# Performance work log

Measured on AMD Instinct MI355X. Metric: run time of the kernel, lower is better.

The kernel has to match this reference:

```python
import jax, jax.numpy as jnp
import numpy as np

B, T, HID = 8, 1024, 1024
N_HEADS, HEAD = 16, HID // 16
MAX_F, BASE = 1024, 10000.0


def _rope_tables():
    inv_freq = 1.0 / (BASE ** (np.arange(0, HEAD, 2, dtype=np.float32) / HEAD))
    t = np.arange(MAX_F, dtype=np.float32)
    freqs = np.einsum('i,j->ij', t, inv_freq)  # (MAX_F, HEAD/2)
    emb = np.concatenate([freqs, freqs], axis=-1)  # (MAX_F, HEAD)
    return jnp.asarray(np.cos(emb)), jnp.asarray(np.sin(emb))


def setup_inputs() -> dict:
    key = jax.random.key(0)
    ks = jax.random.split(key, 6)
    x = jax.random.normal(ks[0], (B, T, HID), dtype=jnp.float32)
    Wq = jax.random.normal(ks[1], (HID, HID), dtype=jnp.float32) * 0.02
    Wk = jax.random.normal(ks[2], (HID, HID), dtype=jnp.float32) * 0.02
    Wv = jax.random.normal(ks[3], (HID, HID), dtype=jnp.float32) * 0.02
    Wo = jax.random.normal(ks[4], (HID, HID), dtype=jnp.float32) * 0.02
    cos, sin = _rope_tables()
    attn_mask = jnp.ones((B, T, T), dtype=jnp.int32)
    timestamp = jax.random.randint(ks[5], (B, T), 0, MAX_F, dtype=jnp.int32)
    return {"x": x, "Wq": Wq, "Wk": Wk, "Wv": Wv, "Wo": Wo,
            "cos": cos, "sin": sin, "attn_mask": attn_mask, "timestamp": timestamp}


def _rotate_half(u):
    u1, u2 = u[..., : HEAD // 2], u[..., HEAD // 2:]
    return jnp.concatenate([-u2, u1], axis=-1)


def reference(x, Wq, Wk, Wv, Wo, cos, sin, attn_mask, timestamp):
    Bx, Tx, _ = x.shape
    # QKV projections (nn.Linear: x @ W.T), reshape to (B, H, T, head)
    def proj(W):
        return (x @ W.T).reshape(Bx, Tx, N_HEADS, HEAD).transpose(0, 2, 1, 3)
    q, k, v = proj(Wq), proj(Wk), proj(Wv)
    # RoPE: gather cos/sin by timestamp, broadcast over heads (unsqueeze dim 1)
    c = cos[timestamp][:, None]  # (B, 1, T, head)
    s = sin[timestamp][:, None]
    q = q * c + _rotate_half(q) * s
    k = k * c + _rotate_half(k) * s
    # Masked SDPA
    scale = 1.0 / jnp.sqrt(jnp.float32(HEAD))
    scores = jnp.einsum('bhqd,bhkd->bhqk', q, k) * scale
    mask = attn_mask[:, None].astype(bool)  # (B, 1, T, T) broadcasts over heads
    scores = jnp.where(mask, scores, jnp.finfo(scores.dtype).min)
    attn = jax.nn.softmax(scores, axis=-1)
    out = jnp.einsum('bhqk,bhkd->bhqd', attn, v)
    out = out.transpose(0, 2, 1, 3).reshape(Bx, Tx, HID)
    return out @ Wo.T
```

## Files before the change

### kernel.cpp

```cpp
#include <hip/hip_runtime.h>
#include <hip/hip_bf16.h>

#define B_   8
#define T_   1024
#define HID_ 1024
#define NH_  16
#define HD_  64
#define K2   2048

typedef __attribute__((ext_vector_type(8))) short bf16x8;
typedef __attribute__((ext_vector_type(4))) float f32x4;

__device__ __forceinline__ void gl_lds16(const void* g, void* l) {
    __builtin_amdgcn_global_load_lds((const __attribute__((address_space(1))) void*)g,
                                     (__attribute__((address_space(3))) void*)l, 16, 0, 0);
}

__device__ __forceinline__ float fast_exp2(float x) {
    return __builtin_amdgcn_exp2f(x);
}

__global__ __launch_bounds__(256) void prep_fused(const float* __restrict__ x,
                                                  const float* __restrict__ Wq,
                                                  const float* __restrict__ Wk,
                                                  const float* __restrict__ Wv,
                                                  const float* __restrict__ Wo,
                                                  const int* __restrict__ mask,
                                                  __hip_bfloat16* __restrict__ xb,
                                                  __hip_bfloat16* __restrict__ wqkv,
                                                  __hip_bfloat16* __restrict__ wo,
                                                  unsigned long long* __restrict__ mbits) {
    const int bid = blockIdx.x;
    const int tid = threadIdx.x;
    if (bid < 12288) {
        const float* X;
        __hip_bfloat16* Y;
        int lb;
        if (bid < 8192)       { X = x;  Y = xb;                              lb = bid; }
        else if (bid < 9216)  { X = Wq; Y = wqkv;                            lb = bid - 8192; }
        else if (bid < 10240) { X = Wk; Y = wqkv + (size_t)1024 * 1024;      lb = bid - 9216; }
        else if (bid < 11264) { X = Wv; Y = wqkv + (size_t)2048 * 1024;      lb = bid - 10240; }
        else                  { X = Wo; Y = wo;                              lb = bid - 11264; }
        int gid = lb * 256 + tid;
        int f = gid << 2;
        float4 xv = *(const float4*)(X + f);
        union { __hip_bfloat16 b[4]; ushort4 u; } p;
        p.b[0] = __float2bfloat16(xv.x);
        p.b[1] = __float2bfloat16(xv.y);
        p.b[2] = __float2bfloat16(xv.z);
        p.b[3] = __float2bfloat16(xv.w);
        if (bid < 11264) {
            *(ushort4*)(Y + f) = p.u;
        } else {
            int m = f >> 10, kk = f & 1023;
            size_t base = (size_t)m * K2 + kk;
            *(ushort4*)(Y + base) = p.u;
            *(ushort4*)(Y + base + 1024) = p.u;
        }
    } else {
        int gid = (bid - 12288) * 256 + tid;
        int wid = gid >> 6;
        int lane = tid & 63;
        int m = mask[(size_t)wid * 64 + lane];
        unsigned long long bal = __ballot(m != 0);
        if (lane == 0) mbits[wid] = bal;
    }
}

__global__ __launch_bounds__(256) void mask_dense(const unsigned long long* __restrict__ mbits,
                                                  unsigned int* __restrict__ tdense) {
    int gid = blockIdx.x * 256 + threadIdx.x;
    int e = gid >> 6;
    int lane = threadIdx.x & 63;
    int b = e >> 8, qt = (e >> 4) & 15, kt = e & 15;
    unsigned long long val = mbits[((size_t)(b * T_ + qt * 64 + lane)) * 16 + kt];
    unsigned long long bal = __ballot(val == ~0ull);
    if (lane == 0) tdense[e] = (bal == ~0ull) ? 1u : 0u;
}

template<int MODE, int KD>
__global__ __launch_bounds__(256, 4) void gemm_mfma(const __hip_bfloat16* __restrict__ A,
                                                    const __hip_bfloat16* __restrict__ Wp,
                                                    float* __restrict__ C0,
                                                    __hip_bfloat16* __restrict__ qbf,
                                                    __hip_bfloat16* __restrict__ kbf,
                                                    __hip_bfloat16* __restrict__ vt,
                                                    const float* __restrict__ cost,
                                                    const float* __restrict__ sint,
                                                    const int* __restrict__ ts) {
    __shared__ __hip_bfloat16 As[2][128 * 32];
    __shared__ __hip_bfloat16 Bs[2][128 * 32];
    const int tid = threadIdx.x;
    const int lane = tid & 63;
    const int w = tid >> 6;
    const int wm = w >> 1, wn = w & 1;
    const int m0 = blockIdx.y * 128, n0 = blockIdx.x * 128;
    const int r0 = tid >> 2;
    const int ks = (tid & 3) << 3;
    const int ml = lane & 15;
    const int kg = (lane >> 4) << 3;
    const int q4 = (lane >> 4) << 2;

    f32x4 acc[4][4];
#pragma unroll
    for (int i = 0; i < 4; ++i)
#pragma unroll
        for (int j = 0; j < 4; ++j) acc[i][j] = (f32x4){0.f, 0.f, 0.f, 0.f};

    for (int k0 = 0; k0 < KD; k0 += 64) {
#pragma unroll
        for (int c = 0; c < 2; ++c) {
            const int kc = k0 + c * 32 + ks;
            gl_lds16(A  + (size_t)(m0 + r0)      * KD + kc, &As[c][r0 * 32 + ks]);
            gl_lds16(A  + (size_t)(m0 + 64 + r0) * KD + kc, &As[c][(64 + r0) * 32 + ks]);
            gl_lds16(Wp + (size_t)(n0 + r0)      * KD + kc, &Bs[c][r0 * 32 + ks]);
            gl_lds16(Wp + (size_t)(n0 + 64 + r0) * KD + kc, &Bs[c][(64 + r0) * 32 + ks]);
        }
        __syncthreads();

#pragma unroll
        for (int c = 0; c < 2; ++c) {
            bf16x8 a[4], b[4];
#pragma unroll
            for (int mi = 0; mi < 4; ++mi)
                a[mi] = *(const bf16x8*)(&As[c][(wm * 64 + mi * 16 + ml) * 32 + kg]);
#pragma unroll
            for (int ni = 0; ni < 4; ++ni)
                b[ni] = *(const bf16x8*)(&Bs[c][(wn * 64 + ni * 16 + ml) * 32 + kg]);
#pragma unroll
            for (int mi = 0; mi < 4; ++mi)
#pragma unroll
                for (int ni = 0; ni < 4; ++ni)
                    acc[mi][ni] = __builtin_amdgcn_mfma_f32_16x16x32_bf16(a[mi], b[ni], acc[mi][ni], 0, 0, 0);
        }
        __syncthreads();
    }

    if (MODE == 0) {
#pragma unroll
        for (int mi = 0; mi < 4; ++mi)
#pragma unroll
            for (int ni = 0; ni < 4; ++ni) {
                int n = n0 + wn * 64 + ni * 16 + ml;
#pragma unroll
                for (int r = 0; r < 4; ++r) {
                    int m = m0 + wm * 64 + mi * 16 + q4 + r;
                    C0[(size_t)m * 1024 + n] = acc[mi][ni][r];
                }
            }
    } else {
        const int nB = n0 + wn * 64;
        const int sel = nB >> 10;
        const int h = (nB & 1023) >> 6;
        if (sel < 2) {
            __hip_bfloat16* dst = sel ? kbf : qbf;
#pragma unroll
            for (int mi = 0; mi < 4; ++mi) {
#pragma unroll
                for (int r = 0; r < 4; ++r) {
                    int m = m0 + wm * 64 + mi * 16 + q4 + r;
                    int tsv = ts[m];
                    int bb = m >> 10, t = m & 1023;
                    size_t rowoff = ((size_t)(bb * NH_ + h) * T_ + t) * HD_;
#pragma unroll
                    for (int ni = 0; ni < 4; ++ni) {
                        int d = ni * 16 + ml;
                        float c = cost[tsv * HD_ + d];
                        float s = sint[tsv * HD_ + d];
                        float u  = acc[mi][ni][r];
                        float up = acc[mi][ni ^ 2][r];
                        float o = (ni < 2) ? (u * c - up * s) : (u * c + up * s);
                        dst[rowoff + d] = __float2bfloat16(o);
                    }
                }
            }
        } else {
#pragma unroll
            for (int mi = 0; mi < 4; ++mi)
#pragma unroll
                for (int r = 0; r < 4; ++r) {
                    int m = m0 + wm * 64 + mi * 16 + q4 + r;
                    int bb = m >> 10, t = m & 1023;
#pragma unroll
                    for (int ni = 0; ni < 4; ++ni) {
                        int d = ni * 16 + ml;
                        vt[((size_t)(bb * NH_ + h) * HD_ + d) * T_ + t] =
                            __float2bfloat16(acc[mi][ni][r]);
                    }
                }
        }
    }
}

__global__ __launch_bounds__(256, 4) void flash_mfma(const __hip_bfloat16* __restrict__ qg,
                                                     const __hip_bfloat16* __restrict__ kg_,
                                                     const __hip_bfloat16* __restrict__ vtg,
                                                     const unsigned long long* __restrict__ mbits,
                                                     const unsigned int* __restrict__ tdense,
                                                     __hip_bfloat16* __restrict__ xs) {
    __shared__ __hip_bfloat16 Ks[2][64 * 64];
    __shared__ __hip_bfloat16 Vt[2][64 * 64];
    __shared__ __hip_bfloat16 Ps[4][16 * 64];
    const int id = blockIdx.x;
    const int qt = (id >> 3) & 15;
    const int hb = ((id >> 7) << 3) | (id & 7);
    const int h = hb & 15, b = hb >> 4;
    const int tid = threadIdx.x;
    const int lane = tid & 63;
    const int w = tid >> 6;
    const int ml = lane & 15;
    const int g4 = lane >> 4;
    const int kg8 = g4 << 3;
    const int q4 = g4 << 2;
    const int q0 = qt * 64;
    const size_t bh_off = (size_t)(b * NH_ + h) * T_ * HD_;
    const __hip_bfloat16* qb = qg + bh_off;
    const __hip_bfloat16* kb = kg_ + bh_off;
    const __hip_bfloat16* vtb = vtg + bh_off;
    const float SCL = 0.125f * 1.44269504f;

    const int srow = lane >> 3;
    const int sg8 = ((lane & 7) ^ srow) << 3;
    const int sx = ((g4 ^ (ml & 7)) << 4);
    const int pswz = (ml & 7) << 4;

    bf16x8 qf0 = *(const bf16x8*)(qb + (size_t)(q0 + w * 16 + ml) * HD_ + kg8);
    bf16x8 qf1 = *(const bf16x8*)(qb + (size_t)(q0 + w * 16 + ml) * HD_ + 32 + kg8);

    f32x4 acc_o[4];
    float lsum = 0.f;
#pragma unroll
    for (int i = 0; i < 4; ++i) acc_o[i] = (f32x4){0.f, 0.f, 0.f, 0.f};
    char* psw = (char*)&Ps[w][0];

#pragma unroll
    for (int p = 0; p < 2; ++p) {
        const int rbase = p * 32 + w * 8;
        gl_lds16(kb  + (size_t)(rbase + srow) * HD_ + sg8, &Ks[0][rbase * 64]);
        gl_lds16(vtb + (size_t)(rbase + srow) * T_  + sg8, &Vt[0][rbase * 64]);
    }

    for (int kt = 0; kt < 16; ++kt) {
        const int cur = kt & 1;
        __syncthreads();
        if (kt < 15) {
            const int k0n = (kt + 1) * 64;
            const int nb = cur ^ 1;
#pragma unroll
            for (int p = 0; p < 2; ++p) {
                const int rbase = p * 32 + w * 8;
                gl_lds16(kb  + (size_t)(k0n + rbase + srow) * HD_ + sg8, &Ks[nb][rbase * 64]);
                gl_lds16(vtb + (size_t)(rbase + srow) * T_ + k0n + sg8, &Vt[nb][rbase * 64]);
            }
        }

        f32x4 sacc[4];
#pragma unroll
        for (int ni = 0; ni < 4; ++ni) sacc[ni] = (f32x4){0.f, 0.f, 0.f, 0.f};
        const char* ksb = (const char*)&Ks[cur][0];
#pragma unroll
        for (int ni = 0; ni < 4; ++ni) {
            const char* rp = ksb + (ni * 16 + ml) * 128;
            bf16x8 kf0 = *(const bf16x8*)(rp + sx);
            bf16x8 kf1 = *(const bf16x8*)(rp + (sx ^ 64));
            sacc[ni] = __builtin_amdgcn_mfma_f32_16x16x32_bf16(kf0, qf0, sacc[ni], 0, 0, 0);
            sacc[ni] = __builtin_amdgcn_mfma_f32_16x16x32_bf16(kf1, qf1, sacc[ni], 0, 0, 0);
        }

        if (tdense[(b * 16 + qt) * 16 + kt]) {
#pragma unroll
            for (int ni = 0; ni < 4; ++ni) {
                float pv[4];
#pragma unroll
                for (int r = 0; r < 4; ++r) pv[r] = fast_exp2(sacc[ni][r] * SCL);
                lsum += (pv[0] + pv[1]) + (pv[2] + pv[3]);
                union { __hip_bfloat16 bb[4]; unsigned long long u8; } pk;
                pk.bb[0] = __float2bfloat16(pv[0]);
                pk.bb[1] = __float2bfloat16(pv[1]);
                pk.bb[2] = __float2bfloat16(pv[2]);
                pk.bb[3] = __float2bfloat16(pv[3]);
                *(unsigned long long*)(psw + ml * 128 + ((ni * 32 + g4 * 8) ^ pswz)) = pk.u8;
            }
        } else {
            unsigned long long mb =
                mbits[((size_t)(b * T_ + q0 + w * 16 + ml)) * 16 + kt];
#pragma unroll
            for (int ni = 0; ni < 4; ++ni) {
                float pv[4];
#pragma unroll
                for (int r = 0; r < 4; ++r) {
                    int kv = ni * 16 + q4 + r;
                    pv[r] = ((mb >> kv) & 1ull) ? fast_exp2(sacc[ni][r] * SCL) : 0.f;
                }
                lsum += (pv[0] + pv[1]) + (pv[2] + pv[3]);
                union { __hip_bfloat16 bb[4]; unsigned long long u8; } pk;
                pk.bb[0] = __float2bfloat16(pv[0]);
                pk.bb[1] = __float2bfloat16(pv[1]);
                pk.bb[2] = __float2bfloat16(pv[2]);
                pk.bb[3] = __float2bfloat16(pv[3]);
                *(unsigned long long*)(psw + ml * 128 + ((ni * 32 + g4 * 8) ^ pswz)) = pk.u8;
            }
        }

        bf16x8 pf0 = *(const bf16x8*)(psw + ml * 128 + sx);
        bf16x8 pf1 = *(const bf16x8*)(psw + ml * 128 + (sx ^ 64));

        const char* vsb = (const char*)&Vt[cur][0];
#pragma unroll
        for (int dt = 0; dt < 4; ++dt) {
            const char* rp = vsb + (dt * 16 + ml) * 128;
            bf16x8 vf0 = *(const bf16x8*)(rp + sx);
            bf16x8 vf1 = *(const bf16x8*)(rp + (sx ^ 64));
            acc_o[dt] = __builtin_amdgcn_mfma_f32_16x16x32_bf16(pf0, vf0, acc_o[dt], 0, 0, 0);
            acc_o[dt] = __builtin_amdgcn_mfma_f32_16x16x32_bf16(pf1, vf1, acc_o[dt], 0, 0, 0);
        }
    }

    float l = lsum;
    l += __shfl_xor(l, 16);
    l += __shfl_xor(l, 32);
#pragma unroll
    for (int r = 0; r < 4; ++r) {
        float lr = __shfl(l, q4 + r, 16);
        float inv = 1.0f / lr;
        size_t rb = (size_t)(b * T_ + q0 + w * 16 + q4 + r) * K2;
#pragma unroll
        for (int dt = 0; dt < 4; ++dt) {
            float val = acc_o[dt][r] * inv;
            int col = h * HD_ + dt * 16 + ml;
            __hip_bfloat16 hi = __float2bfloat16(val);
            __hip_bfloat16 lo = __float2bfloat16(val - __bfloat162float(hi));
            xs[rb + col] = hi;
            xs[rb + 1024 + col] = lo;
        }
    }
}

extern "C" void kernel_launch(void* const* d_in, const int* in_sizes, int n_in,
                              void* d_out, int out_size, void* d_ws, size_t ws_size,
                              hipStream_t stream) {
    const float* x    = (const float*)d_in[0];
    const float* Wq   = (const float*)d_in[1];
    const float* Wk   = (const float*)d_in[2];
    const float* Wv   = (const float*)d_in[3];
    const float* Wo   = (const float*)d_in[4];
    const float* cost = (const float*)d_in[5];
    const float* sint = (const float*)d_in[6];
    const int*   mask = (const int*)d_in[7];
    const int*   ts   = (const int*)d_in[8];
    float* out = (float*)d_out;

    const size_t MB = 1ull << 20;
    char* wsp = (char*)d_ws;
    __hip_bfloat16* qbf  = (__hip_bfloat16*)(wsp + 0 * MB);
    __hip_bfloat16* kbf  = (__hip_bfloat16*)(wsp + 16 * MB);
    __hip_bfloat16* vt   = (__hip_bfloat16*)(wsp + 32 * MB);
    __hip_bfloat16* xs   = (__hip_bfloat16*)(wsp + 48 * MB);
    __hip_bfloat16* xb   = (__hip_bfloat16*)(wsp + 80 * MB);
    __hip_bfloat16* wqkv = (__hip_bfloat16*)(wsp + 96 * MB);
    __hip_bfloat16* wo   = (__hip_bfloat16*)(wsp + 102 * MB);
    unsigned long long* mbits = (unsigned long long*)(wsp + 106 * MB);
    unsigned int* tdense = (unsigned int*)(wsp + 107 * MB);

    prep_fused<<<45056, 256, 0, stream>>>(x, Wq, Wk, Wv, Wo, mask,
                                          xb, wqkv, wo, mbits);
    mask_dense<<<512, 256, 0, stream>>>(mbits, tdense);

    gemm_mfma<2, 1024><<<dim3(24, 64), 256, 0, stream>>>(xb, wqkv, nullptr,
                                                         qbf, kbf, vt, cost, sint, ts);

    flash_mfma<<<2048, 256, 0, stream>>>(qbf, kbf, vt, mbits, tdense, xs);

    gemm_mfma<0, K2><<<dim3(8, 64), 256, 0, stream>>>(xs, wo, out,
                                                      nullptr, nullptr, nullptr,
                                                      nullptr, nullptr, nullptr);
}
```

Measured before the change: 310.7 us.

## Double-buffer GEMM LDS tiles to overlap global prefetch with MFMA compute

```diff
diff --git a/kernel.cpp b/kernel.cpp
--- a/kernel.cpp
+++ b/kernel.cpp
@@ -107,33 +107,35 @@
 #pragma unroll
         for (int j = 0; j < 4; ++j) acc[i][j] = (f32x4){0.f, 0.f, 0.f, 0.f};
 
-    for (int k0 = 0; k0 < KD; k0 += 64) {
-#pragma unroll
-        for (int c = 0; c < 2; ++c) {
-            const int kc = k0 + c * 32 + ks;
-            gl_lds16(A  + (size_t)(m0 + r0)      * KD + kc, &As[c][r0 * 32 + ks]);
-            gl_lds16(A  + (size_t)(m0 + 64 + r0) * KD + kc, &As[c][(64 + r0) * 32 + ks]);
-            gl_lds16(Wp + (size_t)(n0 + r0)      * KD + kc, &Bs[c][r0 * 32 + ks]);
-            gl_lds16(Wp + (size_t)(n0 + 64 + r0) * KD + kc, &Bs[c][(64 + r0) * 32 + ks]);
-        }
+    gl_lds16(A  + (size_t)(m0 + r0)      * KD + ks, &As[0][r0 * 32 + ks]);
+    gl_lds16(A  + (size_t)(m0 + 64 + r0) * KD + ks, &As[0][(64 + r0) * 32 + ks]);
+    gl_lds16(Wp + (size_t)(n0 + r0)      * KD + ks, &Bs[0][r0 * 32 + ks]);
+    gl_lds16(Wp + (size_t)(n0 + 64 + r0) * KD + ks, &Bs[0][(64 + r0) * 32 + ks]);
+
+    const int NT = KD / 32;
+    for (int t = 0; t < NT; ++t) {
+        const int cur = t & 1;
         __syncthreads();
-
-#pragma unroll
-        for (int c = 0; c < 2; ++c) {
-            bf16x8 a[4], b[4];
-#pragma unroll
-            for (int mi = 0; mi < 4; ++mi)
-                a[mi] = *(const bf16x8*)(&As[c][(wm * 64 + mi * 16 + ml) * 32 + kg]);
+        if (t < NT - 1) {
+            const int kc = (t + 1) * 32 + ks;
+            const int nb = cur ^ 1;
+            gl_lds16(A  + (size_t)(m0 + r0)      * KD + kc, &As[nb][r0 * 32 + ks]);
+            gl_lds16(A  + (size_t)(m0 + 64 + r0) * KD + kc, &As[nb][(64 + r0) * 32 + ks]);
+            gl_lds16(Wp + (size_t)(n0 + r0)      * KD + kc, &Bs[nb][r0 * 32 + ks]);
+            gl_lds16(Wp + (size_t)(n0 + 64 + r0) * KD + kc, &Bs[nb][(64 + r0) * 32 + ks]);
+        }
+        bf16x8 a[4], b[4];
+#pragma unroll
+        for (int mi = 0; mi < 4; ++mi)
+            a[mi] = *(const bf16x8*)(&As[cur][(wm * 64 + mi * 16 + ml) * 32 + kg]);
+#pragma unroll
+        for (int ni = 0; ni < 4; ++ni)
+            b[ni] = *(const bf16x8*)(&Bs[cur][(wn * 64 + ni * 16 + ml) * 32 + kg]);
+#pragma unroll
+        for (int mi = 0; mi < 4; ++mi)
 #pragma unroll
             for (int ni = 0; ni < 4; ++ni)
-                b[ni] = *(const bf16x8*)(&Bs[c][(wn * 64 + ni * 16 + ml) * 32 + kg]);
-#pragma unroll
-            for (int mi = 0; mi < 4; ++mi)
-#pragma unroll
-                for (int ni = 0; ni < 4; ++ni)
-                    acc[mi][ni] = __builtin_amdgcn_mfma_f32_16x16x32_bf16(a[mi], b[ni], acc[mi][ni], 0, 0, 0);
-        }
-        __syncthreads();
+                acc[mi][ni] = __builtin_amdgcn_mfma_f32_16x16x32_bf16(a[mi], b[ni], acc[mi][ni], 0, 0, 0);
     }
 
     if (MODE == 0) {
```

Result: slower. 325.1 us (+4.6%).

## Drop mask_dense kernel, check tile density per wave, widen prep conversion

Applied to the files above, without the earlier changes.

```diff
diff --git a/kernel.cpp b/kernel.cpp
--- a/kernel.cpp
+++ b/kernel.cpp
@@ -32,50 +32,48 @@
                                                   unsigned long long* __restrict__ mbits) {
     const int bid = blockIdx.x;
     const int tid = threadIdx.x;
-    if (bid < 12288) {
+    if (bid < 6144) {
         const float* X;
         __hip_bfloat16* Y;
         int lb;
-        if (bid < 8192)       { X = x;  Y = xb;                              lb = bid; }
-        else if (bid < 9216)  { X = Wq; Y = wqkv;                            lb = bid - 8192; }
-        else if (bid < 10240) { X = Wk; Y = wqkv + (size_t)1024 * 1024;      lb = bid - 9216; }
-        else if (bid < 11264) { X = Wv; Y = wqkv + (size_t)2048 * 1024;      lb = bid - 10240; }
-        else                  { X = Wo; Y = wo;                              lb = bid - 11264; }
+        if (bid < 4096)      { X = x;  Y = xb;                          lb = bid; }
+        else if (bid < 4608) { X = Wq; Y = wqkv;                        lb = bid - 4096; }
+        else if (bid < 5120) { X = Wk; Y = wqkv + (size_t)1024 * 1024;  lb = bid - 4608; }
+        else if (bid < 5632) { X = Wv; Y = wqkv + (size_t)2048 * 1024;  lb = bid - 5120; }
+        else                 { X = Wo; Y = wo;                          lb = bid - 5632; }
         int gid = lb * 256 + tid;
-        int f = gid << 2;
-        float4 xv = *(const float4*)(X + f);
-        union { __hip_bfloat16 b[4]; ushort4 u; } p;
-        p.b[0] = __float2bfloat16(xv.x);
-        p.b[1] = __float2bfloat16(xv.y);
-        p.b[2] = __float2bfloat16(xv.z);
-        p.b[3] = __float2bfloat16(xv.w);
-        if (bid < 11264) {
-            *(ushort4*)(Y + f) = p.u;
+        int f = gid << 3;
+        float4 a0 = *(const float4*)(X + f);
+        float4 a1 = *(const float4*)(X + f + 4);
+        union { __hip_bfloat16 b[8]; bf16x8 v; } p;
+        p.b[0] = __float2bfloat16(a0.x);
+        p.b[1] = __float2bfloat16(a0.y);
+        p.b[2] = __float2bfloat16(a0.z);
+        p.b[3] = __float2bfloat16(a0.w);
+        p.b[4] = __float2bfloat16(a1.x);
+        p.b[5] = __float2bfloat16(a1.y);
+        p.b[6] = __float2bfloat16(a1.z);
+        p.b[7] = __float2bfloat16(a1.w);
+        if (bid < 5632) {
+            *(bf16x8*)(Y + f) = p.v;
         } else {
             int m = f >> 10, kk = f & 1023;
             size_t base = (size_t)m * K2 + kk;
-            *(ushort4*)(Y + base) = p.u;
-            *(ushort4*)(Y + base + 1024) = p.u;
+            *(bf16x8*)(Y + base) = p.v;
+            *(bf16x8*)(Y + base + 1024) = p.v;
         }
     } else {
-        int gid = (bid - 12288) * 256 + tid;
-        int wid = gid >> 6;
-        int lane = tid & 63;
-        int m = mask[(size_t)wid * 64 + lane];
-        unsigned long long bal = __ballot(m != 0);
-        if (lane == 0) mbits[wid] = bal;
-    }
-}
-
-__global__ __launch_bounds__(256) void mask_dense(const unsigned long long* __restrict__ mbits,
-                                                  unsigned int* __restrict__ tdense) {
-    int gid = blockIdx.x * 256 + threadIdx.x;
-    int e = gid >> 6;
-    int lane = threadIdx.x & 63;
-    int b = e >> 8, qt = (e >> 4) & 15, kt = e & 15;
-    unsigned long long val = mbits[((size_t)(b * T_ + qt * 64 + lane)) * 16 + kt];
-    unsigned long long bal = __ballot(val == ~0ull);
-    if (lane == 0) tdense[e] = (bal == ~0ull) ? 1u : 0u;
+        const int blk = bid - 6144;
+        const int w = tid >> 6, lane = tid & 63;
+        const int widbase = blk * 16 + w * 4;
+#pragma unroll
+        for (int j = 0; j < 4; ++j) {
+            int wid = widbase + j;
+            int m = mask[(size_t)wid * 64 + lane];
+            unsigned long long bal = __ballot(m != 0);
+            if (lane == 0) mbits[wid] = bal;
+        }
+    }
 }
 
 template<int MODE, int KD>
@@ -196,7 +194,6 @@
                                                      const __hip_bfloat16* __restrict__ kg_,
                                                      const __hip_bfloat16* __restrict__ vtg,
                                                      const unsigned long long* __restrict__ mbits,
-                                                     const unsigned int* __restrict__ tdense,
                                                      __hip_bfloat16* __restrict__ xs) {
     __shared__ __hip_bfloat16 Ks[2][64 * 64];
     __shared__ __hip_bfloat16 Vt[2][64 * 64];
@@ -267,7 +264,9 @@
             sacc[ni] = __builtin_amdgcn_mfma_f32_16x16x32_bf16(kf1, qf1, sacc[ni], 0, 0, 0);
         }
 
-        if (tdense[(b * 16 + qt) * 16 + kt]) {
+        unsigned long long mb =
+            mbits[((size_t)(b * T_ + q0 + w * 16 + ml)) * 16 + kt];
+        if (__all(mb == ~0ull)) {
 #pragma unroll
             for (int ni = 0; ni < 4; ++ni) {
                 float pv[4];
@@ -282,8 +281,6 @@
                 *(unsigned long long*)(psw + ml * 128 + ((ni * 32 + g4 * 8) ^ pswz)) = pk.u8;
             }
         } else {
-            unsigned long long mb =
-                mbits[((size_t)(b * T_ + q0 + w * 16 + ml)) * 16 + kt];
 #pragma unroll
             for (int ni = 0; ni < 4; ++ni) {
                 float pv[4];
@@ -360,16 +357,14 @@
     __hip_bfloat16* wqkv = (__hip_bfloat16*)(wsp + 96 * MB);
     __hip_bfloat16* wo   = (__hip_bfloat16*)(wsp + 102 * MB);
     unsigned long long* mbits = (unsigned long long*)(wsp + 106 * MB);
-    unsigned int* tdense = (unsigned int*)(wsp + 107 * MB);
-
-    prep_fused<<<45056, 256, 0, stream>>>(x, Wq, Wk, Wv, Wo, mask,
+
+    prep_fused<<<14336, 256, 0, stream>>>(x, Wq, Wk, Wv, Wo, mask,
                                           xb, wqkv, wo, mbits);
-    mask_dense<<<512, 256, 0, stream>>>(mbits, tdense);
 
     gemm_mfma<2, 1024><<<dim3(24, 64), 256, 0, stream>>>(xb, wqkv, nullptr,
                                                          qbf, kbf, vt, cost, sint, ts);
 
-    flash_mfma<<<2048, 256, 0, stream>>>(qbf, kbf, vt, mbits, tdense, xs);
+    flash_mfma<<<2048, 256, 0, stream>>>(qbf, kbf, vt, mbits, xs);
 
     gemm_mfma<0, K2><<<dim3(8, 64), 256, 0, stream>>>(xs, wo, out,
                                                       nullptr, nullptr, nullptr,
```

Result: faster. 299.7 us (-3.5%).
